# Optimization experiments

Hardware: AMD Instinct MI355X
Metric: run time of the kernel (lower is better)

## Reference

```python
import jax, jax.numpy as jnp
import numpy as np

B = 16384
DIM = 1024
HEADS = 16
LN_EPS = 1e-5


def setup_inputs() -> dict:
    key = jax.random.key(0)
    ks = jax.random.split(key, 8)
    d = DIM
    s = 0.02
    return {
        "x_u": jax.random.normal(ks[0], (B, d), dtype=jnp.float32),
        "x_m": jax.random.normal(ks[1], (B, d), dtype=jnp.float32),
        # MHA m2u (path 1): packed in_proj [3d, d] like torch, out_proj [d, d]
        "w_qkv1": (jax.random.normal(ks[2], (3 * d, d), dtype=jnp.float32) * s),
        "b_qkv1": jnp.zeros((3 * d,), dtype=jnp.float32),
        "w_o1": (jax.random.normal(ks[3], (d, d), dtype=jnp.float32) * s),
        "b_o1": jnp.zeros((d,), dtype=jnp.float32),
        # MHA u2m (path 2)
        "w_qkv2": (jax.random.normal(ks[4], (3 * d, d), dtype=jnp.float32) * s),
        "b_qkv2": jnp.zeros((3 * d,), dtype=jnp.float32),
        "w_o2": (jax.random.normal(ks[5], (d, d), dtype=jnp.float32) * s),
        "b_o2": jnp.zeros((d,), dtype=jnp.float32),
        # proj head: LayerNorm(2d) + Linear(2d -> d) + GELU (dropout = eval identity)
        "ln_g": jnp.ones((2 * d,), dtype=jnp.float32),
        "ln_b": jnp.zeros((2 * d,), dtype=jnp.float32),
        "w_proj": (jax.random.normal(ks[6], (d, 2 * d), dtype=jnp.float32) * s),
        "b_proj": jnp.zeros((d,), dtype=jnp.float32),
        "heads": HEADS,
    }


def _mha_single_token(xq, xkv, w_qkv, b_qkv, w_o, b_o, heads):
    # seq_len = 1 cross-attention: softmax over a single key is exactly 1.
    d = xq.shape[-1]
    dh = d // heads
    wq, wk, wv = jnp.split(w_qkv, 3, axis=0)
    bq, bk, bv = jnp.split(b_qkv, 3)
    q = (xq @ wq.T + bq).reshape(-1, heads, dh)   # [B, H, dh]
    k = (xkv @ wk.T + bk).reshape(-1, heads, dh)
    v = (xkv @ wv.T + bv).reshape(-1, heads, dh)
    scores = jnp.sum(q * k, axis=-1) / jnp.sqrt(jnp.asarray(dh, q.dtype))  # [B, H]
    attn = jax.nn.softmax(scores[..., None], axis=-1)  # singleton key axis -> ones
    out = (attn * v).reshape(-1, d)                    # [B, d]
    return out @ w_o.T + b_o


def reference(x_u, x_m, w_qkv1, b_qkv1, w_o1, b_o1,
              w_qkv2, b_qkv2, w_o2, b_o2,
              ln_g, ln_b, w_proj, b_proj, heads):
    # Path 1: Q = x_m, K/V = x_u ; Path 2: Q = x_u, K/V = x_m
    z1 = _mha_single_token(x_m, x_u, w_qkv1, b_qkv1, w_o1, b_o1, heads)
    z2 = _mha_single_token(x_u, x_m, w_qkv2, b_qkv2, w_o2, b_o2, heads)
    z = jnp.concatenate([z1, z2], axis=-1)  # [B, 2d]
    mu = jnp.mean(z, axis=-1, keepdims=True)
    var = jnp.mean(jnp.square(z - mu), axis=-1, keepdims=True)
    zn = (z - mu) * jax.lax.rsqrt(var + LN_EPS) * ln_g + ln_b
    h = zn @ w_proj.T + b_proj               # [B, d]
    return jax.nn.gelu(h, approximate=False)  # torch nn.GELU default = exact erf
```

## Files before the change

kernel.cpp:

```cpp
#include <hip/hip_runtime.h>
#include <cstdint>


#define DIM 1024
#define BROWS 16384

typedef __bf16 bf16x8 __attribute__((ext_vector_type(8)));
typedef float f32x4 __attribute__((ext_vector_type(4)));

__device__ __forceinline__ ushort f2bf(float f) {
    uint32_t u = __builtin_bit_cast(uint32_t, f);
    u = (u + 0x7fffu + ((u >> 16) & 1u)) >> 16;
    return (ushort)u;
}

__device__ __forceinline__ void async_copy16(const void* gsrc, void* ldst) {
    __builtin_amdgcn_global_load_lds(
        (__attribute__((address_space(1))) void*)((uintptr_t)gsrc),
        (__attribute__((address_space(3))) void*)((uint32_t)(uintptr_t)ldst),
        16, 0, 0);
}


__global__ __launch_bounds__(256) void convert_x_kernel(
        const float4* __restrict__ xu, const float4* __restrict__ xm,
        ushort4* __restrict__ out, int n4) {
    int i = blockIdx.x * 256 + threadIdx.x;
    int stride = gridDim.x * 256;
    for (; i < 2 * n4; i += stride) {
        float4 v = (i < n4) ? xu[i] : xm[i - n4];
        ushort4 o;
        o.x = f2bf(v.x); o.y = f2bf(v.y); o.z = f2bf(v.z); o.w = f2bf(v.w);
        out[i] = o;
    }
}

__global__ __launch_bounds__(256) void convert_w_kernel(
        const float4* __restrict__ wo1, const float4* __restrict__ wo2,
        const float4* __restrict__ wproj, const float* __restrict__ lng,
        ushort4* __restrict__ wo12, ushort4* __restrict__ Wp) {
    const int NWO = (DIM * DIM) / 4;
    const int NWP = (DIM * 2 * DIM) / 4;
    int i = blockIdx.x * 256 + threadIdx.x;
    int stride = gridDim.x * 256;
    for (; i < 2 * NWO + NWP; i += stride) {
        if (i < 2 * NWO) {
            float4 v = (i < NWO) ? wo1[i] : wo2[i - NWO];
            ushort4 o;
            o.x = f2bf(v.x); o.y = f2bf(v.y); o.z = f2bf(v.z); o.w = f2bf(v.w);
            wo12[i] = o;
        } else {
            int j = i - 2 * NWO;
            float4 v = wproj[j];
            int c = (j * 4) & (2 * DIM - 1);
            v.x *= lng[c]; v.y *= lng[c + 1]; v.z *= lng[c + 2]; v.w *= lng[c + 3];
            ushort4 o;
            o.x = f2bf(v.x); o.y = f2bf(v.y); o.z = f2bf(v.z); o.w = f2bf(v.w);
            Wp[j] = o;
        }
    }
}

__global__ __launch_bounds__(256) void transpose_wv_kernel(
        const float* __restrict__ wqkv1, const float* __restrict__ wqkv2,
        ushort* __restrict__ wvT12) {
    int i = blockIdx.x * 256 + threadIdx.x;
    if (i >= 2 * DIM * DIM) return;
    int z = i >> 20;
    int r = i & (DIM * DIM - 1);
    int k = r >> 10;
    int m = r & (DIM - 1);
    const float* src = z ? wqkv2 : wqkv1;
    wvT12[i] = f2bf(src[(2 * DIM + m) * DIM + k]);
}

__global__ __launch_bounds__(256) void vecprep_kernel(
        const float* __restrict__ wo1, const float* __restrict__ bqkv1, const float* __restrict__ bo1,
        const float* __restrict__ wo2, const float* __restrict__ bqkv2, const float* __restrict__ bo2,
        const float* __restrict__ wproj, const float* __restrict__ lng,
        const float* __restrict__ lnb, const float* __restrict__ bproj,
        float* __restrict__ b12, float* __restrict__ Svec, float* __restrict__ Cvec) {
    int j = blockIdx.x, t = threadIdx.x;
    float s1 = 0.f, s2 = 0.f, sS = 0.f, sC = 0.f;
    for (int c = t; c < DIM; c += 256) {
        s1 += wo1[j * DIM + c] * bqkv1[2 * DIM + c];
        s2 += wo2[j * DIM + c] * bqkv2[2 * DIM + c];
    }
    for (int c = t; c < 2 * DIM; c += 256) {
        float w = wproj[j * 2 * DIM + c];
        sS += w * lng[c];
        sC += w * lnb[c];
    }
    for (int o = 32; o; o >>= 1) {
        s1 += __shfl_down(s1, o, 64);
        s2 += __shfl_down(s2, o, 64);
        sS += __shfl_down(sS, o, 64);
        sC += __shfl_down(sC, o, 64);
    }
    __shared__ float red[4][4];
    int wid = t >> 6;
    if ((t & 63) == 0) { red[wid][0] = s1; red[wid][1] = s2; red[wid][2] = sS; red[wid][3] = sC; }
    __syncthreads();
    if (t == 0) {
        s1 = red[0][0] + red[1][0] + red[2][0] + red[3][0];
        s2 = red[0][1] + red[1][1] + red[2][1] + red[3][1];
        sS = red[0][2] + red[1][2] + red[2][2] + red[3][2];
        sC = red[0][3] + red[1][3] + red[2][3] + red[3][3];
        b12[j]       = s1 + bo1[j];
        b12[DIM + j] = s2 + bo2[j];
        Svec[j] = sS;
        Cvec[j] = sC + bproj[j];
    }
}

__global__ __launch_bounds__(256) void stats_kernel(
        const ushort* __restrict__ z, float* __restrict__ mu, float* __restrict__ rstd) {
    int row = blockIdx.x, t = threadIdx.x;
    const uint4* zr = (const uint4*)(z + (long)row * 2 * DIM);
    uint4 v = zr[t];
    uint32_t u[4] = {v.x, v.y, v.z, v.w};
    float s = 0.f, q = 0.f;
#pragma unroll
    for (int i = 0; i < 4; i++) {
        float a = __builtin_bit_cast(float, u[i] << 16);
        float b = __builtin_bit_cast(float, u[i] & 0xffff0000u);
        s += a + b;
        q += a * a + b * b;
    }
    for (int o = 32; o; o >>= 1) {
        s += __shfl_down(s, o, 64);
        q += __shfl_down(q, o, 64);
    }
    __shared__ float red[4][2];
    int wid = t >> 6;
    if ((t & 63) == 0) { red[wid][0] = s; red[wid][1] = q; }
    __syncthreads();
    if (t == 0) {
        s = red[0][0] + red[1][0] + red[2][0] + red[3][0];
        q = red[0][1] + red[1][1] + red[2][1] + red[3][1];
        float m = s * (1.f / 2048.f);
        float var = q * (1.f / 2048.f) - m * m;
        mu[row] = m;
        rstd[row] = rsqrtf(var + 1e-5f);
    }
}

template <int BM, int BN, int MODE>
__global__ __launch_bounds__(256, 2) void gemm_bt(
        const ushort* __restrict__ Ag, const ushort* __restrict__ Wg,
        void* __restrict__ Cg, int K, int lda, int ldw, int ldc,
        long sAz, long sWz, long sCz,
        const float* __restrict__ bias,
        const float* __restrict__ Svec, const float* __restrict__ Cvec,
        const float* __restrict__ mu, const float* __restrict__ rstd) {
    constexpr int BK = 32;
    constexpr int MT = BM / 32;
    constexpr int NT = BN / 32;
    __shared__ __align__(16) ushort As[BM * BK];
    __shared__ __align__(16) ushort Bs[BN * BK];
    const int tid = threadIdx.x;
    const int wid = tid >> 6;
    const int lane = tid & 63;
    const int quad = lane >> 4;
    const int l16 = lane & 15;
    const int waveM = wid >> 1, waveN = wid & 1;
    const int zb = blockIdx.z;

    const ushort* A = Ag + zb * sAz + (long)blockIdx.x * BM * lda;
    const ushort* W = Wg + zb * sWz + (long)blockIdx.y * BN * ldw;

    f32x4 acc[MT][NT] = {};

    constexpr int nA = (BM * BK) / (256 * 8);
    constexpr int nB = (BN * BK) / (256 * 8);

    for (int k0 = 0; k0 < K; k0 += BK) {
#pragma unroll
        for (int c = 0; c < nA; c++) {
            int idx = c * 256 + tid;
            const ushort* g = A + (long)(idx >> 2) * lda + k0 + (idx & 3) * 8;
            async_copy16(g, (char*)As + (c * 256 + wid * 64) * 16);
        }
#pragma unroll
        for (int c = 0; c < nB; c++) {
            int idx = c * 256 + tid;
            const ushort* g = W + (long)(idx >> 2) * ldw + k0 + (idx & 3) * 8;
            async_copy16(g, (char*)Bs + (c * 256 + wid * 64) * 16);
        }
        asm volatile("s_waitcnt vmcnt(0)" ::: "memory");
        __syncthreads();

        bf16x8 af[MT], bfg[NT];
#pragma unroll
        for (int im = 0; im < MT; im++)
            af[im] = *(const bf16x8*)(As + (waveM * (BM / 2) + im * 16 + l16) * BK + quad * 8);
#pragma unroll
        for (int in = 0; in < NT; in++)
            bfg[in] = *(const bf16x8*)(Bs + (waveN * (BN / 2) + in * 16 + l16) * BK + quad * 8);
#pragma unroll
        for (int im = 0; im < MT; im++)
#pragma unroll
            for (int in = 0; in < NT; in++)
                acc[im][in] = __builtin_amdgcn_mfma_f32_16x16x32_bf16(
                    af[im], bfg[in], acc[im][in], 0, 0, 0);
        __syncthreads();
    }

    const int gRow0 = blockIdx.x * BM + waveM * (BM / 2) + quad * 4;
    const int gCol0 = blockIdx.y * BN + waveN * (BN / 2) + l16;
    if constexpr (MODE == 0 || MODE == 1) {
        ushort* C = (ushort*)Cg + zb * sCz;
#pragma unroll
        for (int im = 0; im < MT; im++) {
#pragma unroll
            for (int in = 0; in < NT; in++) {
                int col = gCol0 + in * 16;
                float badd = 0.f;
                if constexpr (MODE == 1) badd = bias[zb * DIM + col];
#pragma unroll
                for (int r = 0; r < 4; r++) {
                    int row = gRow0 + im * 16 + r;
                    C[(long)row * ldc + col] = f2bf(acc[im][in][r] + badd);
                }
            }
        }
    } else {
        float* O = (float*)Cg;
#pragma unroll
        for (int im = 0; im < MT; im++) {
#pragma unroll
            for (int r = 0; r < 4; r++) {
                int row = gRow0 + im * 16 + r;
                float m = mu[row], rs = rstd[row];
#pragma unroll
                for (int in = 0; in < NT; in++) {
                    int col = gCol0 + in * 16;
                    float h = rs * (acc[im][in][r] - m * Svec[col]) + Cvec[col];
                    O[(long)row * ldc + col] = 0.5f * h * (1.0f + erff(h * 0.7071067811865475f));
                }
            }
        }
    }
}


extern "C" void kernel_launch(void* const* d_in, const int* in_sizes, int n_in,
                              void* d_out, int out_size, void* d_ws, size_t ws_size,
                              hipStream_t stream) {
    (void)in_sizes; (void)n_in; (void)out_size; (void)ws_size;
    const float* x_u   = (const float*)d_in[0];
    const float* x_m   = (const float*)d_in[1];
    const float* wqkv1 = (const float*)d_in[2];
    const float* bqkv1 = (const float*)d_in[3];
    const float* wo1   = (const float*)d_in[4];
    const float* bo1   = (const float*)d_in[5];
    const float* wqkv2 = (const float*)d_in[6];
    const float* bqkv2 = (const float*)d_in[7];
    const float* wo2   = (const float*)d_in[8];
    const float* bo2   = (const float*)d_in[9];
    const float* lng   = (const float*)d_in[10];
    const float* lnb   = (const float*)d_in[11];
    const float* wproj = (const float*)d_in[12];
    const float* bproj = (const float*)d_in[13];

    char* ws = (char*)d_ws;
    ushort* x_bf  = (ushort*)(ws + 0);
    ushort* wo12  = (ushort*)(ws + 67108864);
    ushort* wvT12 = (ushort*)(ws + 71303168);
    ushort* W12   = (ushort*)(ws + 75497472);
    ushort* Wp    = (ushort*)(ws + 79691776);
    ushort* zbuf  = (ushort*)(ws + 83886080);
    float*  b12   = (float*)(ws + 150994944);
    float*  Svec  = (float*)(ws + 151003136);
    float*  Cvec  = (float*)(ws + 151007232);
    float*  mu    = (float*)(ws + 151011328);
    float*  rstd  = (float*)(ws + 151076864);

    convert_x_kernel<<<8192, 256, 0, stream>>>(
        (const float4*)x_u, (const float4*)x_m, (ushort4*)x_bf, (BROWS * DIM) / 4);
    convert_w_kernel<<<2048, 256, 0, stream>>>(
        (const float4*)wo1, (const float4*)wo2, (const float4*)wproj, lng,
        (ushort4*)wo12, (ushort4*)Wp);
    transpose_wv_kernel<<<8192, 256, 0, stream>>>(wqkv1, wqkv2, wvT12);
    vecprep_kernel<<<1024, 256, 0, stream>>>(
        wo1, bqkv1, bo1, wo2, bqkv2, bo2, wproj, lng, lnb, bproj, b12, Svec, Cvec);

    gemm_bt<64, 64, 0><<<dim3(16, 16, 2), 256, 0, stream>>>(
        wo12, wvT12, W12, DIM, DIM, DIM, DIM,
        (long)DIM * DIM, (long)DIM * DIM, (long)DIM * DIM,
        nullptr, nullptr, nullptr, nullptr, nullptr);

    gemm_bt<128, 128, 1><<<dim3(128, 8, 2), 256, 0, stream>>>(
        x_bf, W12, zbuf, DIM, DIM, DIM, 2 * DIM,
        (long)BROWS * DIM, (long)DIM * DIM, (long)DIM,
        b12, nullptr, nullptr, nullptr, nullptr);

    stats_kernel<<<BROWS, 256, 0, stream>>>(zbuf, mu, rstd);

    gemm_bt<128, 128, 2><<<dim3(128, 8, 1), 256, 0, stream>>>(
        zbuf, Wp, d_out, 2 * DIM, 2 * DIM, 2 * DIM, DIM,
        0, 0, 0,
        nullptr, Svec, Cvec, mu, rstd);
}
```

Measured before the change: 422.0 us.

## Merge prep kernels, fuse LayerNorm stats into GEMM epilogue, swizzle LDS

```diff
diff --git a/kernel.cpp b/kernel.cpp
--- a/kernel.cpp
+++ b/kernel.cpp
@@ -22,126 +22,111 @@
 }
 
 
-__global__ __launch_bounds__(256) void convert_x_kernel(
-        const float4* __restrict__ xu, const float4* __restrict__ xm,
-        ushort4* __restrict__ out, int n4) {
-    int i = blockIdx.x * 256 + threadIdx.x;
-    int stride = gridDim.x * 256;
-    for (; i < 2 * n4; i += stride) {
-        float4 v = (i < n4) ? xu[i] : xm[i - n4];
-        ushort4 o;
-        o.x = f2bf(v.x); o.y = f2bf(v.y); o.z = f2bf(v.z); o.w = f2bf(v.w);
-        out[i] = o;
-    }
-}
-
-__global__ __launch_bounds__(256) void convert_w_kernel(
-        const float4* __restrict__ wo1, const float4* __restrict__ wo2,
-        const float4* __restrict__ wproj, const float* __restrict__ lng,
-        ushort4* __restrict__ wo12, ushort4* __restrict__ Wp) {
-    const int NWO = (DIM * DIM) / 4;
-    const int NWP = (DIM * 2 * DIM) / 4;
-    int i = blockIdx.x * 256 + threadIdx.x;
-    int stride = gridDim.x * 256;
-    for (; i < 2 * NWO + NWP; i += stride) {
-        if (i < 2 * NWO) {
-            float4 v = (i < NWO) ? wo1[i] : wo2[i - NWO];
+__global__ __launch_bounds__(256) void prep_kernel(
+        const float* __restrict__ x_u, const float* __restrict__ x_m,
+        const float* __restrict__ wqkv1, const float* __restrict__ bqkv1,
+        const float* __restrict__ wo1, const float* __restrict__ bo1,
+        const float* __restrict__ wqkv2, const float* __restrict__ bqkv2,
+        const float* __restrict__ wo2, const float* __restrict__ bo2,
+        const float* __restrict__ lng, const float* __restrict__ lnb,
+        const float* __restrict__ wproj, const float* __restrict__ bproj,
+        ushort* __restrict__ x_bf, ushort* __restrict__ wo12,
+        ushort* __restrict__ wvT12, ushort* __restrict__ Wp,
+        float* __restrict__ b12, float* __restrict__ Svec, float* __restrict__ Cvec,
+        float* __restrict__ sums ) {
+    const int b = blockIdx.x, t = threadIdx.x;
+    __shared__ float red[4][4];
+    __shared__ float tls[32][33];
+
+    if (b < 8192) {
+        const int n4 = (BROWS * DIM) / 4;
+        int i = b * 256 + t;
+        const int stride = 8192 * 256;
+        const float4* xu4 = (const float4*)x_u;
+        const float4* xm4 = (const float4*)x_m;
+        ushort4* o4 = (ushort4*)x_bf;
+#pragma unroll
+        for (int it = 0; it < 4; it++, i += stride) {
+            float4 v = (i < n4) ? xu4[i] : xm4[i - n4];
             ushort4 o;
             o.x = f2bf(v.x); o.y = f2bf(v.y); o.z = f2bf(v.z); o.w = f2bf(v.w);
-            wo12[i] = o;
-        } else {
-            int j = i - 2 * NWO;
-            float4 v = wproj[j];
-            int c = (j * 4) & (2 * DIM - 1);
-            v.x *= lng[c]; v.y *= lng[c + 1]; v.z *= lng[c + 2]; v.w *= lng[c + 3];
-            ushort4 o;
-            o.x = f2bf(v.x); o.y = f2bf(v.y); o.z = f2bf(v.z); o.w = f2bf(v.w);
-            Wp[j] = o;
-        }
-    }
-}
-
-__global__ __launch_bounds__(256) void transpose_wv_kernel(
-        const float* __restrict__ wqkv1, const float* __restrict__ wqkv2,
-        ushort* __restrict__ wvT12) {
-    int i = blockIdx.x * 256 + threadIdx.x;
-    if (i >= 2 * DIM * DIM) return;
-    int z = i >> 20;
-    int r = i & (DIM * DIM - 1);
-    int k = r >> 10;
-    int m = r & (DIM - 1);
-    const float* src = z ? wqkv2 : wqkv1;
-    wvT12[i] = f2bf(src[(2 * DIM + m) * DIM + k]);
-}
-
-__global__ __launch_bounds__(256) void vecprep_kernel(
-        const float* __restrict__ wo1, const float* __restrict__ bqkv1, const float* __restrict__ bo1,
-        const float* __restrict__ wo2, const float* __restrict__ bqkv2, const float* __restrict__ bo2,
-        const float* __restrict__ wproj, const float* __restrict__ lng,
-        const float* __restrict__ lnb, const float* __restrict__ bproj,
-        float* __restrict__ b12, float* __restrict__ Svec, float* __restrict__ Cvec) {
-    int j = blockIdx.x, t = threadIdx.x;
-    float s1 = 0.f, s2 = 0.f, sS = 0.f, sC = 0.f;
-    for (int c = t; c < DIM; c += 256) {
-        s1 += wo1[j * DIM + c] * bqkv1[2 * DIM + c];
-        s2 += wo2[j * DIM + c] * bqkv2[2 * DIM + c];
-    }
-    for (int c = t; c < 2 * DIM; c += 256) {
-        float w = wproj[j * 2 * DIM + c];
-        sS += w * lng[c];
-        sC += w * lnb[c];
-    }
-    for (int o = 32; o; o >>= 1) {
-        s1 += __shfl_down(s1, o, 64);
-        s2 += __shfl_down(s2, o, 64);
-        sS += __shfl_down(sS, o, 64);
-        sC += __shfl_down(sC, o, 64);
-    }
-    __shared__ float red[4][4];
-    int wid = t >> 6;
-    if ((t & 63) == 0) { red[wid][0] = s1; red[wid][1] = s2; red[wid][2] = sS; red[wid][3] = sC; }
-    __syncthreads();
-    if (t == 0) {
-        s1 = red[0][0] + red[1][0] + red[2][0] + red[3][0];
-        s2 = red[0][1] + red[1][1] + red[2][1] + red[3][1];
-        sS = red[0][2] + red[1][2] + red[2][2] + red[3][2];
-        sC = red[0][3] + red[1][3] + red[2][3] + red[3][3];
-        b12[j]       = s1 + bo1[j];
-        b12[DIM + j] = s2 + bo2[j];
-        Svec[j] = sS;
-        Cvec[j] = sC + bproj[j];
-    }
-}
-
-__global__ __launch_bounds__(256) void stats_kernel(
-        const ushort* __restrict__ z, float* __restrict__ mu, float* __restrict__ rstd) {
-    int row = blockIdx.x, t = threadIdx.x;
-    const uint4* zr = (const uint4*)(z + (long)row * 2 * DIM);
-    uint4 v = zr[t];
-    uint32_t u[4] = {v.x, v.y, v.z, v.w};
-    float s = 0.f, q = 0.f;
-#pragma unroll
-    for (int i = 0; i < 4; i++) {
-        float a = __builtin_bit_cast(float, u[i] << 16);
-        float b = __builtin_bit_cast(float, u[i] & 0xffff0000u);
-        s += a + b;
-        q += a * a + b * b;
-    }
-    for (int o = 32; o; o >>= 1) {
-        s += __shfl_down(s, o, 64);
-        q += __shfl_down(q, o, 64);
-    }
-    __shared__ float red[4][2];
-    int wid = t >> 6;
-    if ((t & 63) == 0) { red[wid][0] = s; red[wid][1] = q; }
-    __syncthreads();
-    if (t == 0) {
-        s = red[0][0] + red[1][0] + red[2][0] + red[3][0];
-        q = red[0][1] + red[1][1] + red[2][1] + red[3][1];
-        float m = s * (1.f / 2048.f);
-        float var = q * (1.f / 2048.f) - m * m;
-        mu[row] = m;
-        rstd[row] = rsqrtf(var + 1e-5f);
+            o4[i] = o;
+        }
+    } else if (b < 9216) {
+        int j = b - 8192;
+        float s1 = 0.f, s2 = 0.f, sS = 0.f, sC = 0.f;
+        for (int c = t; c < DIM; c += 256) {
+            s1 += wo1[j * DIM + c] * bqkv1[2 * DIM + c];
+            s2 += wo2[j * DIM + c] * bqkv2[2 * DIM + c];
+        }
+        for (int c = t; c < 2 * DIM; c += 256) {
+            float w = wproj[j * 2 * DIM + c];
+            sS += w * lng[c];
+            sC += w * lnb[c];
+        }
+        for (int o = 32; o; o >>= 1) {
+            s1 += __shfl_down(s1, o, 64);
+            s2 += __shfl_down(s2, o, 64);
+            sS += __shfl_down(sS, o, 64);
+            sC += __shfl_down(sC, o, 64);
+        }
+        int wid = t >> 6;
+        if ((t & 63) == 0) { red[wid][0] = s1; red[wid][1] = s2; red[wid][2] = sS; red[wid][3] = sC; }
+        __syncthreads();
+        if (t == 0) {
+            s1 = red[0][0] + red[1][0] + red[2][0] + red[3][0];
+            s2 = red[0][1] + red[1][1] + red[2][1] + red[3][1];
+            sS = red[0][2] + red[1][2] + red[2][2] + red[3][2];
+            sC = red[0][3] + red[1][3] + red[2][3] + red[3][3];
+            b12[j]       = s1 + bo1[j];
+            b12[DIM + j] = s2 + bo2[j];
+            Svec[j] = sS;
+            Cvec[j] = sC + bproj[j];
+        }
+    } else if (b < 12288) {
+        const int NWO = (DIM * DIM) / 4;
+        const int NWP = (DIM * 2 * DIM) / 4;
+        const int total = 2 * NWO + NWP;
+        int i = (b - 9216) * 256 + t;
+        const int stride = 3072 * 256;
+        for (; i < total; i += stride) {
+            if (i < 2 * NWO) {
+                float4 v = (i < NWO) ? ((const float4*)wo1)[i] : ((const float4*)wo2)[i - NWO];
+                ushort4 o;
+                o.x = f2bf(v.x); o.y = f2bf(v.y); o.z = f2bf(v.z); o.w = f2bf(v.w);
+                ((ushort4*)wo12)[i] = o;
+            } else {
+                int j = i - 2 * NWO;
+                float4 v = ((const float4*)wproj)[j];
+                int c = (j * 4) & (2 * DIM - 1);
+                v.x *= lng[c]; v.y *= lng[c + 1]; v.z *= lng[c + 2]; v.w *= lng[c + 3];
+                ushort4 o;
+                o.x = f2bf(v.x); o.y = f2bf(v.y); o.z = f2bf(v.z); o.w = f2bf(v.w);
+                ((ushort4*)Wp)[j] = o;
+            }
+        }
+    } else if (b < 14336) {
+        int tile = b - 12288;
+        int z = tile >> 10;
+        int t2 = tile & 1023;
+        int mt = t2 >> 5, kt = t2 & 31;
+        const float* src = z ? wqkv2 : wqkv1;
+        int tr = t >> 3;
+        int tc4 = (t & 7) * 4;
+        const float* p = src + (long)(2 * DIM + mt * 32 + tr) * DIM + kt * 32 + tc4;
+        float4 v = *(const float4*)p;
+        tls[tr][tc4 + 0] = v.x; tls[tr][tc4 + 1] = v.y;
+        tls[tr][tc4 + 2] = v.z; tls[tr][tc4 + 3] = v.w;
+        __syncthreads();
+        ushort4 o;
+        o.x = f2bf(tls[tc4 + 0][tr]);
+        o.y = f2bf(tls[tc4 + 1][tr]);
+        o.z = f2bf(tls[tc4 + 2][tr]);
+        o.w = f2bf(tls[tc4 + 3][tr]);
+        *(ushort4*)(wvT12 + (long)z * DIM * DIM + (long)(kt * 32 + tr) * DIM + mt * 32 + tc4) = o;
+    } else {
+        int i = (b - 14336) * 256 + t;
+        ((float4*)sums)[i] = float4{0.f, 0.f, 0.f, 0.f};
     }
 }
 
@@ -152,7 +137,7 @@
         long sAz, long sWz, long sCz,
         const float* __restrict__ bias,
         const float* __restrict__ Svec, const float* __restrict__ Cvec,
-        const float* __restrict__ mu, const float* __restrict__ rstd) {
+        float* __restrict__ sumbuf, float* __restrict__ sqbuf) {
     constexpr int BK = 32;
     constexpr int MT = BM / 32;
     constexpr int NT = BN / 32;
@@ -174,17 +159,23 @@
     constexpr int nA = (BM * BK) / (256 * 8);
     constexpr int nB = (BN * BK) / (256 * 8);
 
+    const int swz = (l16 >> 1) & 3;
+    const int rdA = quad ^ swz;
     for (int k0 = 0; k0 < K; k0 += BK) {
 #pragma unroll
         for (int c = 0; c < nA; c++) {
             int idx = c * 256 + tid;
-            const ushort* g = A + (long)(idx >> 2) * lda + k0 + (idx & 3) * 8;
+            int r = idx >> 2;
+            int q = (idx & 3) ^ ((r >> 1) & 3);
+            const ushort* g = A + (long)r * lda + k0 + q * 8;
             async_copy16(g, (char*)As + (c * 256 + wid * 64) * 16);
         }
 #pragma unroll
         for (int c = 0; c < nB; c++) {
             int idx = c * 256 + tid;
-            const ushort* g = W + (long)(idx >> 2) * ldw + k0 + (idx & 3) * 8;
+            int r = idx >> 2;
+            int q = (idx & 3) ^ ((r >> 1) & 3);
+            const ushort* g = W + (long)r * ldw + k0 + q * 8;
             async_copy16(g, (char*)Bs + (c * 256 + wid * 64) * 16);
         }
         asm volatile("s_waitcnt vmcnt(0)" ::: "memory");
@@ -193,10 +184,10 @@
         bf16x8 af[MT], bfg[NT];
 #pragma unroll
         for (int im = 0; im < MT; im++)
-            af[im] = *(const bf16x8*)(As + (waveM * (BM / 2) + im * 16 + l16) * BK + quad * 8);
+            af[im] = *(const bf16x8*)(As + (waveM * (BM / 2) + im * 16 + l16) * BK + rdA * 8);
 #pragma unroll
         for (int in = 0; in < NT; in++)
-            bfg[in] = *(const bf16x8*)(Bs + (waveN * (BN / 2) + in * 16 + l16) * BK + quad * 8);
+            bfg[in] = *(const bf16x8*)(Bs + (waveN * (BN / 2) + in * 16 + l16) * BK + rdA * 8);
 #pragma unroll
         for (int im = 0; im < MT; im++)
 #pragma unroll
@@ -208,38 +199,72 @@
 
     const int gRow0 = blockIdx.x * BM + waveM * (BM / 2) + quad * 4;
     const int gCol0 = blockIdx.y * BN + waveN * (BN / 2) + l16;
-    if constexpr (MODE == 0 || MODE == 1) {
+    if constexpr (MODE == 0) {
         ushort* C = (ushort*)Cg + zb * sCz;
 #pragma unroll
-        for (int im = 0; im < MT; im++) {
+        for (int im = 0; im < MT; im++)
 #pragma unroll
             for (int in = 0; in < NT; in++) {
                 int col = gCol0 + in * 16;
-                float badd = 0.f;
-                if constexpr (MODE == 1) badd = bias[zb * DIM + col];
 #pragma unroll
                 for (int r = 0; r < 4; r++) {
                     int row = gRow0 + im * 16 + r;
-                    C[(long)row * ldc + col] = f2bf(acc[im][in][r] + badd);
-                }
-            }
-        }
+                    C[(long)row * ldc + col] = f2bf(acc[im][in][r]);
+                }
+            }
+    } else if constexpr (MODE == 1) {
+        ushort* C = (ushort*)Cg + zb * sCz;
+        float rs[MT][4] = {};
+        float rq[MT][4] = {};
+#pragma unroll
+        for (int im = 0; im < MT; im++)
+#pragma unroll
+            for (int in = 0; in < NT; in++) {
+                int col = gCol0 + in * 16;
+                float badd = bias[zb * DIM + col];
+#pragma unroll
+                for (int r = 0; r < 4; r++) {
+                    int row = gRow0 + im * 16 + r;
+                    float val = acc[im][in][r] + badd;
+                    C[(long)row * ldc + col] = f2bf(val);
+                    rs[im][r] += val;
+                    rq[im][r] += val * val;
+                }
+            }
+#pragma unroll
+        for (int im = 0; im < MT; im++)
+#pragma unroll
+            for (int r = 0; r < 4; r++) {
+                float s = rs[im][r], q = rq[im][r];
+#pragma unroll
+                for (int o = 1; o < 16; o <<= 1) {
+                    s += __shfl_xor(s, o, 64);
+                    q += __shfl_xor(q, o, 64);
+                }
+                if (l16 == 0) {
+                    int row = gRow0 + im * 16 + r;
+                    atomicAdd(&sumbuf[row], s);
+                    atomicAdd(&sqbuf[row], q);
+                }
+            }
     } else {
         float* O = (float*)Cg;
 #pragma unroll
-        for (int im = 0; im < MT; im++) {
+        for (int im = 0; im < MT; im++)
 #pragma unroll
             for (int r = 0; r < 4; r++) {
                 int row = gRow0 + im * 16 + r;
-                float m = mu[row], rs = rstd[row];
+                float sv = sumbuf[row], qv = sqbuf[row];
+                float m = sv * (1.f / 2048.f);
+                float var = qv * (1.f / 2048.f) - m * m;
+                float rstd = rsqrtf(var + 1e-5f);
 #pragma unroll
                 for (int in = 0; in < NT; in++) {
                     int col = gCol0 + in * 16;
-                    float h = rs * (acc[im][in][r] - m * Svec[col]) + Cvec[col];
+                    float h = rstd * (acc[im][in][r] - m * Svec[col]) + Cvec[col];
                     O[(long)row * ldc + col] = 0.5f * h * (1.0f + erff(h * 0.7071067811865475f));
                 }
             }
-        }
     }
 }
 
@@ -273,17 +298,13 @@
     float*  b12   = (float*)(ws + 150994944);
     float*  Svec  = (float*)(ws + 151003136);
     float*  Cvec  = (float*)(ws + 151007232);
-    float*  mu    = (float*)(ws + 151011328);
-    float*  rstd  = (float*)(ws + 151076864);
-
-    convert_x_kernel<<<8192, 256, 0, stream>>>(
-        (const float4*)x_u, (const float4*)x_m, (ushort4*)x_bf, (BROWS * DIM) / 4);
-    convert_w_kernel<<<2048, 256, 0, stream>>>(
-        (const float4*)wo1, (const float4*)wo2, (const float4*)wproj, lng,
-        (ushort4*)wo12, (ushort4*)Wp);
-    transpose_wv_kernel<<<8192, 256, 0, stream>>>(wqkv1, wqkv2, wvT12);
-    vecprep_kernel<<<1024, 256, 0, stream>>>(
-        wo1, bqkv1, bo1, wo2, bqkv2, bo2, wproj, lng, lnb, bproj, b12, Svec, Cvec);
+    float*  sumbuf= (float*)(ws + 151011328);
+    float*  sqbuf = (float*)(ws + 151076864);
+
+    prep_kernel<<<14368, 256, 0, stream>>>(
+        x_u, x_m, wqkv1, bqkv1, wo1, bo1, wqkv2, bqkv2, wo2, bo2,
+        lng, lnb, wproj, bproj,
+        x_bf, wo12, wvT12, Wp, b12, Svec, Cvec, sumbuf);
 
     gemm_bt<64, 64, 0><<<dim3(16, 16, 2), 256, 0, stream>>>(
         wo12, wvT12, W12, DIM, DIM, DIM, DIM,
@@ -293,12 +314,10 @@
     gemm_bt<128, 128, 1><<<dim3(128, 8, 2), 256, 0, stream>>>(
         x_bf, W12, zbuf, DIM, DIM, DIM, 2 * DIM,
         (long)BROWS * DIM, (long)DIM * DIM, (long)DIM,
-        b12, nullptr, nullptr, nullptr, nullptr);
-
-    stats_kernel<<<BROWS, 256, 0, stream>>>(zbuf, mu, rstd);
+        b12, nullptr, nullptr, sumbuf, sqbuf);
 
     gemm_bt<128, 128, 2><<<dim3(128, 8, 1), 256, 0, stream>>>(
         zbuf, Wp, d_out, 2 * DIM, 2 * DIM, 2 * DIM, DIM,
         0, 0, 0,
-        nullptr, Svec, Cvec, mu, rstd);
-}
+        nullptr, Svec, Cvec, sumbuf, sqbuf);
+}
```

New measurement: 404.2 us. 4.2% less time.
